# Kernel tuning notes

Measured on AMD Instinct MI355X. Metric: run time of the kernel, lower is better.

## Reference

```python
import jax, jax.numpy as jnp
import numpy as np

N_NODES = 50000
N_EDGES = 500000
H = 128          # h_dim
HEADS = 3
B = 512          # histories with non-zero length
L = 10           # seq_len (all histories full length)
N_RELS = 200
NEG_SLOPE = 0.2  # DGL GATConv default negative_slope


def setup_inputs() -> dict:
    key = jax.random.key(0)
    ks = jax.random.split(key, 18)
    p = lambda i, shape: jax.random.normal(ks[i], shape, jnp.float32) * 0.05
    return {
        "node_feat": jax.random.normal(ks[0], (N_NODES, H), jnp.float32),
        "W1": p(1, (H, HEADS * H)),
        "attn_l1": p(2, (HEADS, H)),
        "attn_r1": p(3, (HEADS, H)),
        "b1": p(4, (HEADS * H,)),
        "W2": p(5, (H, HEADS * H)),
        "attn_l2": p(6, (HEADS, H)),
        "attn_r2": p(7, (HEADS, H)),
        "b2": p(8, (HEADS * H,)),
        "ent_embeds": jax.random.normal(ks[9], (N_NODES, H), jnp.float32),
        "rel_embeds": jax.random.normal(ks[10], (N_RELS, H), jnp.float32),
        "global_emb_list": jax.random.normal(ks[11], (B * L, H), jnp.float32),
        "s_hist_t": jax.random.uniform(ks[12], (B, L), jnp.float32),
        "edge_src": jax.random.randint(ks[13], (N_EDGES,), 0, N_NODES),
        "edge_dst": jax.random.randint(ks[14], (N_EDGES,), 0, N_NODES),
        "node_ids_graph": jax.random.randint(ks[15], (B * L,), 0, N_NODES),
        "s_tem": jax.random.randint(ks[16], (B,), 0, N_NODES),
        "r_tem": jax.random.randint(ks[17], (B,), 0, N_RELS),
    }


def gat_conv(x, W, attn_l, attn_r, bias, src, dst):
    """DGL-style GATConv (allow_zero_in_degree=True, eval mode)."""
    n = x.shape[0]
    feat = (x @ W).reshape(n, HEADS, H)                    # [N, heads, H]
    el = jnp.einsum('nhd,hd->nh', feat, attn_l)            # [N, heads]
    er = jnp.einsum('nhd,hd->nh', feat, attn_r)
    e = jax.nn.leaky_relu(el[src] + er[dst], NEG_SLOPE)    # [E, heads]
    # edge softmax over incoming edges of each dst node
    emax = jax.ops.segment_max(e, dst, num_segments=n)
    ex = jnp.exp(e - emax[dst])
    denom = jax.ops.segment_sum(ex, dst, num_segments=n)
    alpha = ex / denom[dst]                                # [E, heads]
    msg = alpha[:, :, None] * feat[src]                    # [E, heads, H]
    rst = jax.ops.segment_sum(msg, dst, num_segments=n)    # [N, heads, H]
    return rst + bias.reshape(1, HEADS, H)


def reference(node_feat, W1, attn_l1, attn_r1, b1, W2, attn_l2, attn_r2, b2,
              ent_embeds, rel_embeds, global_emb_list, s_hist_t,
              edge_src, edge_dst, node_ids_graph, s_tem, r_tem):
    h = gat_conv(node_feat, W1, attn_l1, attn_r1, b1, edge_src, edge_dst).mean(axis=1)
    h = gat_conv(h, W2, attn_l2, attn_r2, b2, edge_src, edge_dst).mean(axis=1)
    embeds = h[node_ids_graph].reshape(B, L, H)            # gathered history node embeds
    ent = jnp.broadcast_to(ent_embeds[s_tem][:, None, :], (B, L, H))
    rel = jnp.broadcast_to(rel_embeds[r_tem][:, None, :], (B, L, H))
    glob = global_emb_list.reshape(B, L, H)
    seq = jnp.concatenate([embeds, ent, rel, glob], axis=-1)   # [B, L, 4H]
    seq_r = jnp.concatenate([embeds, ent, glob], axis=-1)      # [B, L, 3H]
    return seq, seq_r, s_hist_t
```

## Files before the change

kernel.cpp:

```cpp
#include <hip/hip_runtime.h>
#include <hip/hip_bf16.h>

#define N_NODES 50000
#define N_EDGES 500000
#define HDIM 128
#define HEADS 3
#define BB 512
#define LL 10
#define NEG_SLOPE 0.2f

typedef __hip_bfloat16 bf16;
typedef unsigned char fp8t;
typedef __bf16 v8bf __attribute__((ext_vector_type(8)));
typedef float f32x4 __attribute__((ext_vector_type(4)));


__global__ void k_zero2(int* a, int na, int* b, int nb){
  int i = blockIdx.x*256 + threadIdx.x;
  if(i < na) a[i] = 0;
  if(i < nb) b[i] = 0;
}

__global__ void k_hist(const int* __restrict__ dst, int* __restrict__ cnt, int E){
  int e = blockIdx.x*256 + threadIdx.x;
  if(e < E) atomicAdd(&cnt[dst[e]], 1);
}


#define SCAN_TILE 2048
#define SCAN_NB ((N_NODES + SCAN_TILE - 1)/SCAN_TILE)

__global__ __launch_bounds__(256) void k_scan_part(const int* __restrict__ cnt,
                                                   int* __restrict__ bsum){
  int b = blockIdx.x, tid = threadIdx.x;
  int i0 = b*SCAN_TILE + tid*8;
  int s = 0;
  #pragma unroll
  for(int j = 0; j < 8; ++j){ int i = i0 + j; s += (i < N_NODES) ? cnt[i] : 0; }
  for(int m = 32; m; m >>= 1) s += __shfl_xor(s, m);
  __shared__ int ws[4];
  if((tid & 63) == 0) ws[tid >> 6] = s;
  __syncthreads();
  if(tid == 0) bsum[b] = ws[0] + ws[1] + ws[2] + ws[3];
}

__global__ __launch_bounds__(64) void k_scan_top(int* __restrict__ bsum, int nb){
  int tid = threadIdx.x;
  int v = (tid < nb) ? bsum[tid] : 0;
  for(int s = 1; s < 64; s <<= 1){
    int t = __shfl_up(v, s);
    if(tid >= s) v += t;
  }
  if(tid < nb) bsum[tid] = v;
}

__global__ __launch_bounds__(256) void k_scan_write(int* __restrict__ cnt,
                                                    const int* __restrict__ bsum,
                                                    int* __restrict__ offs){
  int b = blockIdx.x, tid = threadIdx.x;
  int lane = tid & 63, wv = tid >> 6;
  int i0 = b*SCAN_TILE + tid*8;
  int v[8]; int s = 0;
  #pragma unroll
  for(int j = 0; j < 8; ++j){
    int i = i0 + j;
    v[j] = (i < N_NODES) ? cnt[i] : 0;
    s += v[j];
  }
  #pragma unroll
  for(int j = 0; j < 8; ++j){ int i = i0 + j; if(i < N_NODES) cnt[i] = 0; }
  int incl = s;
  for(int sh = 1; sh < 64; sh <<= 1){
    int t = __shfl_up(incl, sh);
    if(lane >= sh) incl += t;
  }
  __shared__ int wtot[4];
  if(lane == 63) wtot[wv] = incl;
  __syncthreads();
  int woff = 0;
  for(int w = 0; w < wv; ++w) woff += wtot[w];
  int excl = woff + incl - s;
  int run = ((b > 0) ? bsum[b-1] : 0) + excl;
  #pragma unroll
  for(int j = 0; j < 8; ++j){
    int i = i0 + j;
    run += v[j];
    if(i < N_NODES) offs[i+1] = run;
  }
  if(b == 0 && tid == 0) offs[0] = 0;
}

__global__ void k_scatter(const int* __restrict__ src, const int* __restrict__ dst,
                          const int* __restrict__ offs, int* __restrict__ cur,
                          int* __restrict__ csr, int E){
  int e = blockIdx.x*256 + threadIdx.x;
  if(e < E){
    int d = dst[e];
    int p = offs[d] + atomicAdd(&cur[d], 1);
    if(p >= 0 && p < E) csr[p] = src[e];
  }
}


__global__ __launch_bounds__(64) void k_mark(const int* __restrict__ nid,
                                             const int* __restrict__ offs,
                                             const int* __restrict__ csr,
                                             unsigned char* __restrict__ mark){
  unsigned n = (unsigned)nid[blockIdx.x];
  if(n >= N_NODES) return;
  if(threadIdx.x == 0) mark[n] = 1;
  int o0 = offs[n], o1 = offs[n+1];
  for(int j = o0 + (int)threadIdx.x; j < o1; j += 64){
    unsigned s = (unsigned)csr[j];
    if(s < N_NODES) mark[s] = 1;
  }
}


__global__ void k_wt(const float* __restrict__ W, bf16* __restrict__ Wt){
  int i = blockIdx.x*256 + threadIdx.x;
  if(i < HEADS*HDIM*HDIM){
    int n = i >> 7, k = i & 127;
    Wt[i] = __float2bfloat16(W[k*(HEADS*HDIM) + n]);
  }
}


template<int AF32>
__global__ __launch_bounds__(256) void k_gemm(const void* __restrict__ Av,
                                              const bf16* __restrict__ Wt,
                                              const float* __restrict__ al,
                                              const float* __restrict__ ar,
                                              fp8t* __restrict__ feat8,
                                              float* __restrict__ el4,
                                              float* __restrict__ er4, int M){
  int tid  = threadIdx.x;
  int wave = tid >> 6, lane = tid & 63;
  int wr = wave >> 1, wc = wave & 1;
  int row0 = blockIdx.x*64 + wr*32;
  int col0 = blockIdx.y*128 + wc*64;
  int l15 = lane & 15, lhi = lane >> 4;

  f32x4 acc[2][4] = {};
  for(int kk = 0; kk < 4; ++kk){
    int kb = kk*32 + lhi*8;
    v8bf a[2], b[4];
    for(int mi = 0; mi < 2; ++mi){
      int r = row0 + mi*16 + l15;
      if(r >= M) r = M - 1;
      if constexpr(AF32){
        const float* ap = (const float*)Av + (size_t)r*HDIM + kb;
        f32x4 lo = *reinterpret_cast<const f32x4*>(ap);
        f32x4 hi = *reinterpret_cast<const f32x4*>(ap + 4);
        #pragma unroll
        for(int j = 0; j < 4; ++j){ a[mi][j] = (__bf16)lo[j]; a[mi][4+j] = (__bf16)hi[j]; }
      } else {
        a[mi] = *reinterpret_cast<const v8bf*>((const bf16*)Av + (size_t)r*HDIM + kb);
      }
    }
    for(int ni = 0; ni < 4; ++ni){
      int c = col0 + ni*16 + l15;
      b[ni] = *reinterpret_cast<const v8bf*>(Wt + (size_t)c*HDIM + kb);
    }
    for(int mi = 0; mi < 2; ++mi)
      for(int ni = 0; ni < 4; ++ni)
        acc[mi][ni] = __builtin_amdgcn_mfma_f32_16x16x32_bf16(a[mi], b[ni], acc[mi][ni], 0, 0, 0);
  }

  const float* alh = al + blockIdx.y*HDIM;
  const float* arh = ar + blockIdx.y*HDIM;
  float alv[4], arv[4];
  #pragma unroll
  for(int ni = 0; ni < 4; ++ni){
    int d = wc*64 + ni*16 + l15;
    alv[ni] = alh[d]; arv[ni] = arh[d];
  }
  __shared__ float red[2][64][2];
  __shared__ int4 tile4[512];
  fp8t* tile8 = (fp8t*)tile4;

  #pragma unroll
  for(int mi = 0; mi < 2; ++mi){
    #pragma unroll
    for(int j = 0; j < 4; ++j){
      float pe = 0.f, pr = 0.f;
      #pragma unroll
      for(int ni = 0; ni < 4; ++ni){
        pe += acc[mi][ni][j]*alv[ni];
        pr += acc[mi][ni][j]*arv[ni];
      }
      for(int k = 8; k; k >>= 1){ pe += __shfl_xor(pe, k); pr += __shfl_xor(pr, k); }
      int row_l = wr*32 + mi*16 + lhi*4 + j;
      if(l15 == 0){ red[wc][row_l][0] = pe; red[wc][row_l][1] = pr; }
    }
  }
  #pragma unroll
  for(int mi = 0; mi < 2; ++mi)
    #pragma unroll
    for(int j = 0; j < 4; ++j){
      int row_l = wr*32 + mi*16 + lhi*4 + j;
      #pragma unroll
      for(int ni = 0; ni < 4; ++ni){
        float x = acc[mi][ni][j];
        unsigned bb = (unsigned)__builtin_amdgcn_cvt_pk_fp8_f32(x, x, 0, false) & 0xFFu;
        tile8[row_l*128 + wc*64 + ni*16 + l15] = (fp8t)bb;
      }
    }
  __syncthreads();

  if(tid < 64){
    int r = blockIdx.x*64 + tid;
    if(r < M){
      el4[(size_t)r*4 + blockIdx.y] = red[0][tid][0] + red[1][tid][0];
      er4[(size_t)r*4 + blockIdx.y] = red[0][tid][1] + red[1][tid][1];
    }
  }
  #pragma unroll
  for(int pass = 0; pass < 2; ++pass){
    int off = pass*4096 + tid*16;
    int row_l = off >> 7, col = off & 127;
    int r = blockIdx.x*64 + row_l;
    if(r < M)
      *reinterpret_cast<int4*>(feat8 + (size_t)r*(HEADS*HDIM) + blockIdx.y*HDIM + col) =
          tile4[off >> 4];
  }
}


__device__ __forceinline__ float lrelu(float x){ return x > 0.f ? x : NEG_SLOPE*x; }

template<int USE_LIST, int USE_MARK>
__global__ __launch_bounds__(256) void k_denom(const float* __restrict__ el4,
                                               const float* __restrict__ er4,
                                               const int* __restrict__ offs,
                                               const int* __restrict__ csr,
                                               const int* __restrict__ list,
                                               const unsigned char* __restrict__ mark,
                                               float* __restrict__ inv4, int total){
  int i = blockIdx.x*256 + threadIdx.x;
  if(i >= total) return;
  unsigned n = USE_LIST ? (unsigned)list[i] : (unsigned)i;
  if(n >= N_NODES) return;
  if(USE_MARK){ if(!mark[n]) return; }
  int o0 = offs[n];
  int deg = offs[n+1] - o0;
  if(deg < 0 || deg > N_EDGES) deg = 0;
  float4 erv = *reinterpret_cast<const float4*>(er4 + (size_t)n*4);
  float S0 = 0.f, S1 = 0.f, S2 = 0.f;
  for(int j = 0; j < deg; ++j){
    unsigned s = (unsigned)csr[o0 + j];
    if(s >= N_NODES) s = 0;
    float4 elv = *reinterpret_cast<const float4*>(el4 + (size_t)s*4);
    S0 += __expf(lrelu(elv.x + erv.x));
    S1 += __expf(lrelu(elv.y + erv.y));
    S2 += __expf(lrelu(elv.z + erv.z));
  }
  float4 iv;
  iv.x = (S0 > 0.f) ? 1.f/S0 : 0.f;
  iv.y = (S1 > 0.f) ? 1.f/S1 : 0.f;
  iv.z = (S2 > 0.f) ? 1.f/S2 : 0.f;
  iv.w = 0.f;
  *reinterpret_cast<float4*>(inv4 + (size_t)n*4) = iv;
}


#define AGG_CHUNK 128
#define SEQ_SZ   (BB*LL*4*HDIM)
#define SEQR_OFF SEQ_SZ
#define SEQR_SZ  (BB*LL*3*HDIM)
#define SH_OFF   (SEQ_SZ + SEQR_SZ)

template<int USE_LIST, int FUSED, int USE_MARK>
__global__ __launch_bounds__(128) void k_agg(const fp8t* __restrict__ feat8,
                                             const float* __restrict__ el4,
                                             const float* __restrict__ er4,
                                             const float* __restrict__ inv4,
                                             const float* __restrict__ bias,
                                             const int* __restrict__ offs,
                                             const int* __restrict__ csr,
                                             const int* __restrict__ list,
                                             const unsigned char* __restrict__ mark,
                                             bf16* __restrict__ h1,
                                             const float* __restrict__ ent_e,
                                             const float* __restrict__ rel_e,
                                             const float* __restrict__ glob,
                                             const float* __restrict__ sht,
                                             const int* __restrict__ s_tem,
                                             const int* __restrict__ r_tem,
                                             float* __restrict__ out){
  int bid = blockIdx.x;
  int n = USE_LIST ? list[bid] : bid;
  if(USE_MARK){ if(!mark[n]) return; }
  int tid = threadIdx.x;
  __shared__ float s_alpha[AGG_CHUNK][4];
  __shared__ int   s_src[AGG_CHUNK];
  __shared__ float s_facc[HEADS*HDIM];
  int o0 = offs[n];
  int deg = offs[n+1] - o0;
  if(deg < 0 || deg > N_EDGES) deg = 0;
  float4 erv = *reinterpret_cast<const float4*>(er4 + (size_t)n*4);
  float4 iv  = *reinterpret_cast<const float4*>(inv4 + (size_t)n*4);

  float a0 = 0.f, a1 = 0.f, a2 = 0.f, a3 = 0.f;
  int head = tid >> 5;
  for(int base = 0; base < deg; base += AGG_CHUNK){
    int cn = min(AGG_CHUNK, deg - base);
    if(base) __syncthreads();
    if(tid < cn){
      unsigned su = (unsigned)csr[o0 + base + tid];
      if(su >= N_NODES) su = 0;
      float4 elv = *reinterpret_cast<const float4*>(el4 + (size_t)su*4);
      s_src[tid] = (int)su;
      s_alpha[tid][0] = __expf(lrelu(elv.x + erv.x))*iv.x;
      s_alpha[tid][1] = __expf(lrelu(elv.y + erv.y))*iv.y;
      s_alpha[tid][2] = __expf(lrelu(elv.z + erv.z))*iv.z;
    }
    __syncthreads();
    if(tid < 96){
      for(int i = 0; i < cn; ++i){
        unsigned u = *reinterpret_cast<const unsigned*>(
            feat8 + (size_t)s_src[i]*(HEADS*HDIM) + tid*4);
        float al = s_alpha[i][head];
        a0 += al*__builtin_amdgcn_cvt_f32_fp8((int)u, 0);
        a1 += al*__builtin_amdgcn_cvt_f32_fp8((int)u, 1);
        a2 += al*__builtin_amdgcn_cvt_f32_fp8((int)u, 2);
        a3 += al*__builtin_amdgcn_cvt_f32_fp8((int)u, 3);
      }
    }
  }
  if(tid < 96){
    float4 w; w.x = a0; w.y = a1; w.z = a2; w.w = a3;
    *reinterpret_cast<float4*>(s_facc + tid*4) = w;
  }
  __syncthreads();
  float r = (s_facc[tid] + s_facc[HDIM + tid] + s_facc[2*HDIM + tid]
           + bias[tid] + bias[HDIM + tid] + bias[2*HDIM + tid])*(1.f/3.f);
  if(FUSED){
    int p = bid, b = p/LL, d = tid;
    float ent = ent_e[(size_t)s_tem[b]*HDIM + d];
    float rel = rel_e[(size_t)r_tem[b]*HDIM + d];
    float gl  = glob[(size_t)p*HDIM + d];
    size_t so = (size_t)p*(4*HDIM);
    out[so + d] = r; out[so + HDIM + d] = ent;
    out[so + 2*HDIM + d] = rel; out[so + 3*HDIM + d] = gl;
    size_t ro = SEQR_OFF + (size_t)p*(3*HDIM);
    out[ro + d] = r; out[ro + HDIM + d] = ent; out[ro + 2*HDIM + d] = gl;
    if(d == 0) out[SH_OFF + p] = sht[p];
  } else {
    h1[(size_t)n*HDIM + tid] = __float2bfloat16(r);
  }
}


extern "C" void kernel_launch(void* const* d_in, const int* in_sizes, int n_in,
                              void* d_out, int out_size, void* d_ws, size_t ws_size,
                              hipStream_t stream){
  const float* node_feat = (const float*)d_in[0];
  const float* W1        = (const float*)d_in[1];
  const float* attn_l1   = (const float*)d_in[2];
  const float* attn_r1   = (const float*)d_in[3];
  const float* b1        = (const float*)d_in[4];
  const float* W2        = (const float*)d_in[5];
  const float* attn_l2   = (const float*)d_in[6];
  const float* attn_r2   = (const float*)d_in[7];
  const float* b2        = (const float*)d_in[8];
  const float* ent_emb   = (const float*)d_in[9];
  const float* rel_emb   = (const float*)d_in[10];
  const float* glob      = (const float*)d_in[11];
  const float* sht       = (const float*)d_in[12];
  const int*  e_src      = (const int*)d_in[13];
  const int*  e_dst      = (const int*)d_in[14];
  const int*  nid        = (const int*)d_in[15];
  const int*  s_tem      = (const int*)d_in[16];
  const int*  r_tem      = (const int*)d_in[17];
  float* out = (float*)d_out;

  char* ws = (char*)d_ws;
  size_t cur_off = 0;
  auto alloc = [&](size_t bytes)->char*{
    char* r = ws + cur_off;
    cur_off += (bytes + 255) & ~(size_t)255;
    return r;
  };
  fp8t*  feat8 = (fp8t*) alloc((size_t)N_NODES*HEADS*HDIM);
  bf16*  h1    = (bf16*) alloc((size_t)N_NODES*HDIM*2);
  float* el4   = (float*)alloc((size_t)N_NODES*4*4);
  float* er4   = (float*)alloc((size_t)N_NODES*4*4);
  float* inv4  = (float*)alloc((size_t)N_NODES*4*4);
  bf16*  wt1   = (bf16*) alloc((size_t)HEADS*HDIM*HDIM*2);
  bf16*  wt2   = (bf16*) alloc((size_t)HEADS*HDIM*HDIM*2);
  int*   offs  = (int*)  alloc((size_t)(N_NODES+1)*4);
  int*   cnt   = (int*)  alloc((size_t)N_NODES*4);
  int*   bsum  = (int*)  alloc((size_t)SCAN_NB*4);
  unsigned char* mark = (unsigned char*)alloc((size_t)N_NODES);
  int*   csr   = (int*)  alloc((size_t)N_EDGES*4);

  k_zero2<<<(N_NODES+255)/256, 256, 0, stream>>>(cnt, N_NODES,
                                                 (int*)mark, (N_NODES+3)/4);
  k_hist<<<(N_EDGES+255)/256, 256, 0, stream>>>(e_dst, cnt, N_EDGES);
  k_scan_part<<<SCAN_NB, 256, 0, stream>>>(cnt, bsum);
  k_scan_top<<<1, 64, 0, stream>>>(bsum, SCAN_NB);
  k_scan_write<<<SCAN_NB, 256, 0, stream>>>(cnt, bsum, offs);
  k_scatter<<<(N_EDGES+255)/256, 256, 0, stream>>>(e_src, e_dst, offs, cnt, csr, N_EDGES);
  k_mark<<<BB*LL, 64, 0, stream>>>(nid, offs, csr, mark);

  k_wt<<<(HEADS*HDIM*HDIM+255)/256, 256, 0, stream>>>(W1, wt1);
  k_wt<<<(HEADS*HDIM*HDIM+255)/256, 256, 0, stream>>>(W2, wt2);

  dim3 ggrid((N_NODES + 63)/64, HEADS);

  k_gemm<1><<<ggrid, 256, 0, stream>>>((const void*)node_feat, wt1, attn_l1, attn_r1,
                                       feat8, el4, er4, N_NODES);
  k_denom<0,1><<<(N_NODES+255)/256, 256, 0, stream>>>(el4, er4, offs, csr,
                                                      nullptr, mark, inv4, N_NODES);
  k_agg<0,0,1><<<N_NODES, 128, 0, stream>>>(feat8, el4, er4, inv4, b1, offs, csr,
                                            nullptr, mark, h1,
                                            nullptr, nullptr, nullptr, nullptr,
                                            nullptr, nullptr, nullptr);

  k_gemm<0><<<ggrid, 256, 0, stream>>>((const void*)h1, wt2, attn_l2, attn_r2,
                                       feat8, el4, er4, N_NODES);
  k_denom<1,0><<<(BB*LL+255)/256, 256, 0, stream>>>(el4, er4, offs, csr,
                                                    nid, nullptr, inv4, BB*LL);
  k_agg<1,1,0><<<BB*LL, 128, 0, stream>>>(feat8, el4, er4, inv4, b2, offs, csr,
                                          nid, nullptr, nullptr,
                                          ent_emb, rel_emb, glob, sht,
                                          s_tem, r_tem, out);
}
```

Baseline: 225.5 us.

## Fuse softmax denominator into aggregation, preconvert features to bf16, preload GEMM operands

Removes the separate k_denom kernels. The aggregation kernel now accumulates the softmax denominator per head alongside the weighted sum and normalizes at the end, which avoids a second pass over the CSR and el4 gathers. Adds a standalone fp32-to-bf16 conversion of node_feat so the GEMM has a single bf16 path. The GEMM now loads all A/B operands for every k-step before issuing the MFMAs, to raise memory-level parallelism at the cost of more registers. The extra conversion kernel adds a full read and write of node_feat.

```diff
diff --git a/kernel.cpp b/kernel.cpp
--- a/kernel.cpp
+++ b/kernel.cpp
@@ -24,6 +24,18 @@
 __global__ void k_hist(const int* __restrict__ dst, int* __restrict__ cnt, int E){
   int e = blockIdx.x*256 + threadIdx.x;
   if(e < E) atomicAdd(&cnt[dst[e]], 1);
+}
+
+__global__ void k_cvt(const float* __restrict__ in, bf16* __restrict__ o, int n){
+  int i = (blockIdx.x*256 + threadIdx.x)*8;
+  if(i < n){
+    f32x4 lo = *reinterpret_cast<const f32x4*>(in + i);
+    f32x4 hi = *reinterpret_cast<const f32x4*>(in + i + 4);
+    v8bf v;
+    #pragma unroll
+    for(int j = 0; j < 4; ++j){ v[j] = (__bf16)lo[j]; v[4+j] = (__bf16)hi[j]; }
+    *reinterpret_cast<v8bf*>(o + i) = v;
+  }
 }
 
 
@@ -126,8 +138,7 @@
 }
 
 
-template<int AF32>
-__global__ __launch_bounds__(256) void k_gemm(const void* __restrict__ Av,
+__global__ __launch_bounds__(256) void k_gemm(const bf16* __restrict__ A,
                                               const bf16* __restrict__ Wt,
                                               const float* __restrict__ al,
                                               const float* __restrict__ ar,
@@ -141,31 +152,32 @@
   int col0 = blockIdx.y*128 + wc*64;
   int l15 = lane & 15, lhi = lane >> 4;
 
-  f32x4 acc[2][4] = {};
+  v8bf a[4][2], b[4][4];
+  #pragma unroll
   for(int kk = 0; kk < 4; ++kk){
     int kb = kk*32 + lhi*8;
-    v8bf a[2], b[4];
+    #pragma unroll
     for(int mi = 0; mi < 2; ++mi){
       int r = row0 + mi*16 + l15;
       if(r >= M) r = M - 1;
-      if constexpr(AF32){
-        const float* ap = (const float*)Av + (size_t)r*HDIM + kb;
-        f32x4 lo = *reinterpret_cast<const f32x4*>(ap);
-        f32x4 hi = *reinterpret_cast<const f32x4*>(ap + 4);
-        #pragma unroll
-        for(int j = 0; j < 4; ++j){ a[mi][j] = (__bf16)lo[j]; a[mi][4+j] = (__bf16)hi[j]; }
-      } else {
-        a[mi] = *reinterpret_cast<const v8bf*>((const bf16*)Av + (size_t)r*HDIM + kb);
-      }
-    }
+      a[kk][mi] = *reinterpret_cast<const v8bf*>(A + (size_t)r*HDIM + kb);
+    }
+    #pragma unroll
     for(int ni = 0; ni < 4; ++ni){
       int c = col0 + ni*16 + l15;
-      b[ni] = *reinterpret_cast<const v8bf*>(Wt + (size_t)c*HDIM + kb);
-    }
+      b[kk][ni] = *reinterpret_cast<const v8bf*>(Wt + (size_t)c*HDIM + kb);
+    }
+  }
+
+  f32x4 acc[2][4] = {};
+  #pragma unroll
+  for(int kk = 0; kk < 4; ++kk)
+    #pragma unroll
     for(int mi = 0; mi < 2; ++mi)
+      #pragma unroll
       for(int ni = 0; ni < 4; ++ni)
-        acc[mi][ni] = __builtin_amdgcn_mfma_f32_16x16x32_bf16(a[mi], b[ni], acc[mi][ni], 0, 0, 0);
-  }
+        acc[mi][ni] = __builtin_amdgcn_mfma_f32_16x16x32_bf16(a[kk][mi], b[kk][ni],
+                                                              acc[mi][ni], 0, 0, 0);
 
   const float* alh = al + blockIdx.y*HDIM;
   const float* arh = ar + blockIdx.y*HDIM;
@@ -229,41 +241,6 @@
 
 __device__ __forceinline__ float lrelu(float x){ return x > 0.f ? x : NEG_SLOPE*x; }
 
-template<int USE_LIST, int USE_MARK>
-__global__ __launch_bounds__(256) void k_denom(const float* __restrict__ el4,
-                                               const float* __restrict__ er4,
-                                               const int* __restrict__ offs,
-                                               const int* __restrict__ csr,
-                                               const int* __restrict__ list,
-                                               const unsigned char* __restrict__ mark,
-                                               float* __restrict__ inv4, int total){
-  int i = blockIdx.x*256 + threadIdx.x;
-  if(i >= total) return;
-  unsigned n = USE_LIST ? (unsigned)list[i] : (unsigned)i;
-  if(n >= N_NODES) return;
-  if(USE_MARK){ if(!mark[n]) return; }
-  int o0 = offs[n];
-  int deg = offs[n+1] - o0;
-  if(deg < 0 || deg > N_EDGES) deg = 0;
-  float4 erv = *reinterpret_cast<const float4*>(er4 + (size_t)n*4);
-  float S0 = 0.f, S1 = 0.f, S2 = 0.f;
-  for(int j = 0; j < deg; ++j){
-    unsigned s = (unsigned)csr[o0 + j];
-    if(s >= N_NODES) s = 0;
-    float4 elv = *reinterpret_cast<const float4*>(el4 + (size_t)s*4);
-    S0 += __expf(lrelu(elv.x + erv.x));
-    S1 += __expf(lrelu(elv.y + erv.y));
-    S2 += __expf(lrelu(elv.z + erv.z));
-  }
-  float4 iv;
-  iv.x = (S0 > 0.f) ? 1.f/S0 : 0.f;
-  iv.y = (S1 > 0.f) ? 1.f/S1 : 0.f;
-  iv.z = (S2 > 0.f) ? 1.f/S2 : 0.f;
-  iv.w = 0.f;
-  *reinterpret_cast<float4*>(inv4 + (size_t)n*4) = iv;
-}
-
-
 #define AGG_CHUNK 128
 #define SEQ_SZ   (BB*LL*4*HDIM)
 #define SEQR_OFF SEQ_SZ
@@ -274,7 +251,6 @@
 __global__ __launch_bounds__(128) void k_agg(const fp8t* __restrict__ feat8,
                                              const float* __restrict__ el4,
                                              const float* __restrict__ er4,
-                                             const float* __restrict__ inv4,
                                              const float* __restrict__ bias,
                                              const int* __restrict__ offs,
                                              const int* __restrict__ csr,
@@ -299,9 +275,8 @@
   int deg = offs[n+1] - o0;
   if(deg < 0 || deg > N_EDGES) deg = 0;
   float4 erv = *reinterpret_cast<const float4*>(er4 + (size_t)n*4);
-  float4 iv  = *reinterpret_cast<const float4*>(inv4 + (size_t)n*4);
-
-  float a0 = 0.f, a1 = 0.f, a2 = 0.f, a3 = 0.f;
+
+  float a0 = 0.f, a1 = 0.f, a2 = 0.f, a3 = 0.f, dh = 0.f;
   int head = tid >> 5;
   for(int base = 0; base < deg; base += AGG_CHUNK){
     int cn = min(AGG_CHUNK, deg - base);
@@ -311,9 +286,9 @@
       if(su >= N_NODES) su = 0;
       float4 elv = *reinterpret_cast<const float4*>(el4 + (size_t)su*4);
       s_src[tid] = (int)su;
-      s_alpha[tid][0] = __expf(lrelu(elv.x + erv.x))*iv.x;
-      s_alpha[tid][1] = __expf(lrelu(elv.y + erv.y))*iv.y;
-      s_alpha[tid][2] = __expf(lrelu(elv.z + erv.z))*iv.z;
+      s_alpha[tid][0] = __expf(lrelu(elv.x + erv.x));
+      s_alpha[tid][1] = __expf(lrelu(elv.y + erv.y));
+      s_alpha[tid][2] = __expf(lrelu(elv.z + erv.z));
     }
     __syncthreads();
     if(tid < 96){
@@ -321,6 +296,7 @@
         unsigned u = *reinterpret_cast<const unsigned*>(
             feat8 + (size_t)s_src[i]*(HEADS*HDIM) + tid*4);
         float al = s_alpha[i][head];
+        dh += al;
         a0 += al*__builtin_amdgcn_cvt_f32_fp8((int)u, 0);
         a1 += al*__builtin_amdgcn_cvt_f32_fp8((int)u, 1);
         a2 += al*__builtin_amdgcn_cvt_f32_fp8((int)u, 2);
@@ -329,7 +305,8 @@
     }
   }
   if(tid < 96){
-    float4 w; w.x = a0; w.y = a1; w.z = a2; w.w = a3;
+    float inv = (dh > 0.f) ? 1.f/dh : 0.f;
+    float4 w; w.x = a0*inv; w.y = a1*inv; w.z = a2*inv; w.w = a3*inv;
     *reinterpret_cast<float4*>(s_facc + tid*4) = w;
   }
   __syncthreads();
@@ -383,10 +360,10 @@
     return r;
   };
   fp8t*  feat8 = (fp8t*) alloc((size_t)N_NODES*HEADS*HDIM);
+  bf16*  nfb   = (bf16*) alloc((size_t)N_NODES*HDIM*2);
   bf16*  h1    = (bf16*) alloc((size_t)N_NODES*HDIM*2);
   float* el4   = (float*)alloc((size_t)N_NODES*4*4);
   float* er4   = (float*)alloc((size_t)N_NODES*4*4);
-  float* inv4  = (float*)alloc((size_t)N_NODES*4*4);
   bf16*  wt1   = (bf16*) alloc((size_t)HEADS*HDIM*HDIM*2);
   bf16*  wt2   = (bf16*) alloc((size_t)HEADS*HDIM*HDIM*2);
   int*   offs  = (int*)  alloc((size_t)(N_NODES+1)*4);
@@ -406,23 +383,20 @@
 
   k_wt<<<(HEADS*HDIM*HDIM+255)/256, 256, 0, stream>>>(W1, wt1);
   k_wt<<<(HEADS*HDIM*HDIM+255)/256, 256, 0, stream>>>(W2, wt2);
+  k_cvt<<<(N_NODES*HDIM/8+255)/256, 256, 0, stream>>>(node_feat, nfb, N_NODES*HDIM);
 
   dim3 ggrid((N_NODES + 63)/64, HEADS);
 
-  k_gemm<1><<<ggrid, 256, 0, stream>>>((const void*)node_feat, wt1, attn_l1, attn_r1,
-                                       feat8, el4, er4, N_NODES);
-  k_denom<0,1><<<(N_NODES+255)/256, 256, 0, stream>>>(el4, er4, offs, csr,
-                                                      nullptr, mark, inv4, N_NODES);
-  k_agg<0,0,1><<<N_NODES, 128, 0, stream>>>(feat8, el4, er4, inv4, b1, offs, csr,
+  k_gemm<<<ggrid, 256, 0, stream>>>(nfb, wt1, attn_l1, attn_r1,
+                                    feat8, el4, er4, N_NODES);
+  k_agg<0,0,1><<<N_NODES, 128, 0, stream>>>(feat8, el4, er4, b1, offs, csr,
                                             nullptr, mark, h1,
                                             nullptr, nullptr, nullptr, nullptr,
                                             nullptr, nullptr, nullptr);
 
-  k_gemm<0><<<ggrid, 256, 0, stream>>>((const void*)h1, wt2, attn_l2, attn_r2,
-                                       feat8, el4, er4, N_NODES);
-  k_denom<1,0><<<(BB*LL+255)/256, 256, 0, stream>>>(el4, er4, offs, csr,
-                                                    nid, nullptr, inv4, BB*LL);
-  k_agg<1,1,0><<<BB*LL, 128, 0, stream>>>(feat8, el4, er4, inv4, b2, offs, csr,
+  k_gemm<<<ggrid, 256, 0, stream>>>(h1, wt2, attn_l2, attn_r2,
+                                    feat8, el4, er4, N_NODES);
+  k_agg<1,1,0><<<BB*LL, 128, 0, stream>>>(feat8, el4, er4, b2, offs, csr,
                                           nid, nullptr, nullptr,
                                           ent_emb, rel_emb, glob, sht,
                                           s_tem, r_tem, out);
```

New measurement: 197.4 us. 12.5% less time.
